# Kernel tuning notes

Hardware: AMD Instinct MI355X
Metric: run time of the kernel (lower is better)

The kernel has to match this reference:

```python
import jax, jax.numpy as jnp
import numpy as np

B, N, D, H = 2, 28, 128, 8
DK = D // H  # 16


def setup_inputs() -> dict:
    key0 = jax.random.key(0)
    ks = jax.random.split(key0, 10)
    query = jax.random.normal(ks[0], (B, N, N, D), dtype=jnp.float32)
    key = jax.random.normal(ks[1], (B, N, N, D), dtype=jnp.float32)
    value = jax.random.normal(ks[2], (B, N, N, D), dtype=jnp.float32)
    mask = jax.random.randint(ks[3], (B, N, N, N), 0, 2).astype(bool)
    scale = 1.0 / np.sqrt(D)
    # six bias-free Linear(d_model, d_model) weights (torch layout: y = x @ W.T)
    Wlk = jax.random.normal(ks[4], (D, D), dtype=jnp.float32) * scale
    Wrk = jax.random.normal(ks[5], (D, D), dtype=jnp.float32) * scale
    Wlv = jax.random.normal(ks[6], (D, D), dtype=jnp.float32) * scale
    Wrv = jax.random.normal(ks[7], (D, D), dtype=jnp.float32) * scale
    Wq = jax.random.normal(ks[8], (D, D), dtype=jnp.float32) * scale
    Wout = jax.random.normal(ks[9], (D, D), dtype=jnp.float32) * scale
    return {"query": query, "key": key, "value": value, "mask": mask,
            "Wlk": Wlk, "Wrk": Wrk, "Wlv": Wlv, "Wrv": Wrv, "Wq": Wq, "Wout": Wout}


def reference(query, key, value, mask, Wlk, Wrk, Wlv, Wrv, Wq, Wout):
    b, n = key.shape[0], key.shape[1]

    def proj(x, W):
        # torch nn.Linear(bias=False): x @ W.T, then view to heads
        return (x @ W.T).reshape(b, n, n, H, DK)

    left_k = proj(key, Wlk)
    right_k = proj(key, Wrk)
    left_v = proj(value, Wlv)
    right_v = proj(value, Wrv)
    # note: linears[4](key) (the 'query' projection, Wq) is computed in the
    # original but unused when lesion_scores=False; omitted (same math).

    # scores[b,x,a,y,h] = <left_k[b,x,a,h,:], right_k[b,a,y,h,:]> / sqrt(d_k)
    scores = jnp.einsum('bxahd,bayhd->bxayh', left_k, right_k) / np.float32(np.sqrt(DK))
    scores = jnp.where(mask[..., None], jnp.float32(-1e9), scores)
    att = jax.nn.softmax(scores, axis=2)  # softmax over intermediate node a
    # dropout p=0.0 -> identity
    # x[b,x,y,h,d] = sum_a att[b,x,a,y,h] * left_v[b,x,a,h,d] * right_v[b,a,y,h,d]
    x = jnp.einsum('bxayh,bxahd,bayhd->bxyhd', att, left_v, right_v)
    x = x.reshape(b, n, n, D)
    return x @ Wout.T
```

## Files before the change

### kernel.cpp

```cpp
#include <hip/hip_runtime.h>

#define B_ 2
#define N_ 28
#define D_ 128
#define H_ 8
#define DK_ 16
#define R_ (B_ * N_ * N_)
#define ROWS_PER_BLK 8

__global__ __launch_bounds__(128) void proj4_kernel(
    const float* __restrict__ key, const float* __restrict__ value,
    const float* __restrict__ Wlk, const float* __restrict__ Wrk,
    const float* __restrict__ Wlv, const float* __restrict__ Wrv,
    float* __restrict__ ws) {
  const int p = blockIdx.y;
  const float* X = (p < 2) ? key : value;
  const float* W = (p == 0) ? Wlk : (p == 1) ? Wrk : (p == 2) ? Wlv : Wrv;
  float* Y = ws + (size_t)p * R_ * D_;

  const int r0 = blockIdx.x * ROWS_PER_BLK;
  const int c = threadIdx.x;

  __shared__ float xs[ROWS_PER_BLK][D_];
#pragma unroll
  for (int i = 0; i < ROWS_PER_BLK; ++i)
    xs[i][c] = X[(size_t)(r0 + i) * D_ + c];
  __syncthreads();

  const float4* w4 = reinterpret_cast<const float4*>(W + (size_t)c * D_);
  float acc[ROWS_PER_BLK];
#pragma unroll
  for (int i = 0; i < ROWS_PER_BLK; ++i) acc[i] = 0.f;

#pragma unroll
  for (int k = 0; k < D_ / 4; ++k) {
    const float4 wv = w4[k];
#pragma unroll
    for (int i = 0; i < ROWS_PER_BLK; ++i) {
      const float4 xv = reinterpret_cast<const float4*>(xs[i])[k];
      acc[i] += xv.x * wv.x + xv.y * wv.y + xv.z * wv.z + xv.w * wv.w;
    }
  }

#pragma unroll
  for (int i = 0; i < ROWS_PER_BLK; ++i)
    Y[(size_t)(r0 + i) * D_ + c] = acc[i];
}

__global__ __launch_bounds__(128) void attn_kernel(
    const float* __restrict__ ws, const int* __restrict__ mask,
    float* __restrict__ xout) {
  const float* lk = ws;
  const float* rk = ws + (size_t)1 * R_ * D_;
  const float* lv = ws + (size_t)2 * R_ * D_;
  const float* rv = ws + (size_t)3 * R_ * D_;

  const int bxy = blockIdx.x;
  const int y = bxy % N_;
  const int bx = bxy / N_;
  const int b = bx / N_;
  const int tid = threadIdx.x;

  const int rowL = bx * N_;
  const int rowR = b * N_ * N_ + y;

  float s[N_];
#pragma unroll
  for (int a = 0; a < N_; ++a) {
    float pr = lk[(size_t)(rowL + a) * D_ + tid] *
               rk[(size_t)(rowR + a * N_) * D_ + tid];
    pr += __shfl_xor(pr, 1);
    pr += __shfl_xor(pr, 2);
    pr += __shfl_xor(pr, 4);
    pr += __shfl_xor(pr, 8);
    s[a] = pr * 0.25f;
  }

  const int* mrow = mask + (size_t)rowL * N_ + y;
#pragma unroll
  for (int a = 0; a < N_; ++a)
    if (mrow[(size_t)a * N_] != 0) s[a] = -1e9f;

  float mx = -3.0e38f;
#pragma unroll
  for (int a = 0; a < N_; ++a) mx = fmaxf(mx, s[a]);
  float den = 0.f;
#pragma unroll
  for (int a = 0; a < N_; ++a) {
    s[a] = __expf(s[a] - mx);
    den += s[a];
  }
  const float inv = 1.0f / den;

  float xv = 0.f;
#pragma unroll
  for (int a = 0; a < N_; ++a) {
    xv += s[a] * lv[(size_t)(rowL + a) * D_ + tid] *
          rv[(size_t)(rowR + a * N_) * D_ + tid];
  }
  xout[(size_t)bxy * D_ + tid] = xv * inv;
}

__global__ __launch_bounds__(128) void gemm_out_kernel(
    const float* __restrict__ X, const float* __restrict__ W,
    float* __restrict__ Y) {
  const int r0 = blockIdx.x * ROWS_PER_BLK;
  const int c = threadIdx.x;

  __shared__ float xs[ROWS_PER_BLK][D_];
#pragma unroll
  for (int i = 0; i < ROWS_PER_BLK; ++i)
    xs[i][c] = X[(size_t)(r0 + i) * D_ + c];
  __syncthreads();

  const float4* w4 = reinterpret_cast<const float4*>(W + (size_t)c * D_);
  float acc[ROWS_PER_BLK];
#pragma unroll
  for (int i = 0; i < ROWS_PER_BLK; ++i) acc[i] = 0.f;

#pragma unroll
  for (int k = 0; k < D_ / 4; ++k) {
    const float4 wv = w4[k];
#pragma unroll
    for (int i = 0; i < ROWS_PER_BLK; ++i) {
      const float4 xv = reinterpret_cast<const float4*>(xs[i])[k];
      acc[i] += xv.x * wv.x + xv.y * wv.y + xv.z * wv.z + xv.w * wv.w;
    }
  }

#pragma unroll
  for (int i = 0; i < ROWS_PER_BLK; ++i)
    Y[(size_t)(r0 + i) * D_ + c] = acc[i];
}

extern "C" void kernel_launch(void* const* d_in, const int* in_sizes, int n_in,
                              void* d_out, int out_size, void* d_ws,
                              size_t ws_size, hipStream_t stream) {
  const float* key = (const float*)d_in[1];
  const float* value = (const float*)d_in[2];
  const int* mask = (const int*)d_in[3];
  const float* Wlk = (const float*)d_in[4];
  const float* Wrk = (const float*)d_in[5];
  const float* Wlv = (const float*)d_in[6];
  const float* Wrv = (const float*)d_in[7];
  const float* Wout = (const float*)d_in[9];
  float* out = (float*)d_out;

  float* ws = (float*)d_ws;
  float* xbuf = ws + (size_t)4 * R_ * D_;

  proj4_kernel<<<dim3(R_ / ROWS_PER_BLK, 4), 128, 0, stream>>>(
      key, value, Wlk, Wrk, Wlv, Wrv, ws);
  attn_kernel<<<dim3(R_), 128, 0, stream>>>(ws, mask, xbuf);
  gemm_out_kernel<<<dim3(R_ / ROWS_PER_BLK), 128, 0, stream>>>(xbuf, Wout, out);
}
```

Before: 33.56 us.

## Fuse attention with output projection and reuse left rows across y group

Merges the attention kernel and the output GEMM into one kernel, so the intermediate x buffer never goes to global memory and one launch is removed. Each block now handles four y values for one (b,x), staging left_k and left_v rows in shared memory once and reusing them. The output projection is done per row, with each thread reading a full Wout row from global memory for every y, and two block barriers per y. The grid shrinks from 1568 to 392 blocks, which lowers parallelism.

```diff
diff --git a/kernel.cpp b/kernel.cpp
--- a/kernel.cpp
+++ b/kernel.cpp
@@ -7,6 +7,7 @@
 #define DK_ 16
 #define R_ (B_ * N_ * N_)
 #define ROWS_PER_BLK 8
+#define YG_ 4
 
 __global__ __launch_bounds__(128) void proj4_kernel(
     const float* __restrict__ key, const float* __restrict__ value,
@@ -47,90 +48,84 @@
     Y[(size_t)(r0 + i) * D_ + c] = acc[i];
 }
 
-__global__ __launch_bounds__(128) void attn_kernel(
+__global__ __launch_bounds__(128) void attn_out_kernel(
     const float* __restrict__ ws, const int* __restrict__ mask,
-    float* __restrict__ xout) {
+    const float* __restrict__ Wout, float* __restrict__ out) {
   const float* lk = ws;
   const float* rk = ws + (size_t)1 * R_ * D_;
   const float* lv = ws + (size_t)2 * R_ * D_;
   const float* rv = ws + (size_t)3 * R_ * D_;
 
-  const int bxy = blockIdx.x;
-  const int y = bxy % N_;
-  const int bx = bxy / N_;
+  const int yg = blockIdx.x % (N_ / YG_);
+  const int bx = blockIdx.x / (N_ / YG_);
   const int b = bx / N_;
   const int tid = threadIdx.x;
 
   const int rowL = bx * N_;
-  const int rowR = b * N_ * N_ + y;
 
-  float s[N_];
+  __shared__ float s_lk[N_][D_];
+  __shared__ float s_lv[N_][D_];
+  __shared__ float s_x[D_];
+
 #pragma unroll
   for (int a = 0; a < N_; ++a) {
-    float pr = lk[(size_t)(rowL + a) * D_ + tid] *
-               rk[(size_t)(rowR + a * N_) * D_ + tid];
-    pr += __shfl_xor(pr, 1);
-    pr += __shfl_xor(pr, 2);
-    pr += __shfl_xor(pr, 4);
-    pr += __shfl_xor(pr, 8);
-    s[a] = pr * 0.25f;
+    s_lk[a][tid] = lk[(size_t)(rowL + a) * D_ + tid];
+    s_lv[a][tid] = lv[(size_t)(rowL + a) * D_ + tid];
   }
-
-  const int* mrow = mask + (size_t)rowL * N_ + y;
-#pragma unroll
-  for (int a = 0; a < N_; ++a)
-    if (mrow[(size_t)a * N_] != 0) s[a] = -1e9f;
-
-  float mx = -3.0e38f;
-#pragma unroll
-  for (int a = 0; a < N_; ++a) mx = fmaxf(mx, s[a]);
-  float den = 0.f;
-#pragma unroll
-  for (int a = 0; a < N_; ++a) {
-    s[a] = __expf(s[a] - mx);
-    den += s[a];
-  }
-  const float inv = 1.0f / den;
-
-  float xv = 0.f;
-#pragma unroll
-  for (int a = 0; a < N_; ++a) {
-    xv += s[a] * lv[(size_t)(rowL + a) * D_ + tid] *
-          rv[(size_t)(rowR + a * N_) * D_ + tid];
-  }
-  xout[(size_t)bxy * D_ + tid] = xv * inv;
-}
-
-__global__ __launch_bounds__(128) void gemm_out_kernel(
-    const float* __restrict__ X, const float* __restrict__ W,
-    float* __restrict__ Y) {
-  const int r0 = blockIdx.x * ROWS_PER_BLK;
-  const int c = threadIdx.x;
-
-  __shared__ float xs[ROWS_PER_BLK][D_];
-#pragma unroll
-  for (int i = 0; i < ROWS_PER_BLK; ++i)
-    xs[i][c] = X[(size_t)(r0 + i) * D_ + c];
   __syncthreads();
 
-  const float4* w4 = reinterpret_cast<const float4*>(W + (size_t)c * D_);
-  float acc[ROWS_PER_BLK];
+  const float4* wrow = reinterpret_cast<const float4*>(Wout + (size_t)tid * D_);
+
+  for (int j = 0; j < YG_; ++j) {
+    const int y = yg * YG_ + j;
+    const int rowR = b * N_ * N_ + y;
+
+    float s[N_];
 #pragma unroll
-  for (int i = 0; i < ROWS_PER_BLK; ++i) acc[i] = 0.f;
+    for (int a = 0; a < N_; ++a) {
+      float pr = s_lk[a][tid] * rk[(size_t)(rowR + a * N_) * D_ + tid];
+      pr += __shfl_xor(pr, 1);
+      pr += __shfl_xor(pr, 2);
+      pr += __shfl_xor(pr, 4);
+      pr += __shfl_xor(pr, 8);
+      s[a] = pr * 0.25f;
+    }
 
+    const int* mrow = mask + (size_t)rowL * N_ + y;
 #pragma unroll
-  for (int k = 0; k < D_ / 4; ++k) {
-    const float4 wv = w4[k];
+    for (int a = 0; a < N_; ++a)
+      if (mrow[(size_t)a * N_] != 0) s[a] = -1e9f;
+
+    float mx = -3.0e38f;
 #pragma unroll
-    for (int i = 0; i < ROWS_PER_BLK; ++i) {
-      const float4 xv = reinterpret_cast<const float4*>(xs[i])[k];
-      acc[i] += xv.x * wv.x + xv.y * wv.y + xv.z * wv.z + xv.w * wv.w;
+    for (int a = 0; a < N_; ++a) mx = fmaxf(mx, s[a]);
+    float den = 0.f;
+#pragma unroll
+    for (int a = 0; a < N_; ++a) {
+      s[a] = __expf(s[a] - mx);
+      den += s[a];
     }
+    const float inv = 1.0f / den;
+
+    float xv = 0.f;
+#pragma unroll
+    for (int a = 0; a < N_; ++a) {
+      xv += s[a] * s_lv[a][tid] * rv[(size_t)(rowR + a * N_) * D_ + tid];
+    }
+    s_x[tid] = xv * inv;
+    __syncthreads();
+
+    float acc = 0.f;
+    const float4* x4 = reinterpret_cast<const float4*>(s_x);
+#pragma unroll
+    for (int k = 0; k < D_ / 4; ++k) {
+      const float4 xk = x4[k];
+      const float4 wv = wrow[k];
+      acc += xk.x * wv.x + xk.y * wv.y + xk.z * wv.z + xk.w * wv.w;
+    }
+    out[(size_t)(rowL + y) * D_ + tid] = acc;
+    __syncthreads();
   }
-
-#pragma unroll
-  for (int i = 0; i < ROWS_PER_BLK; ++i)
-    Y[(size_t)(r0 + i) * D_ + c] = acc[i];
 }
 
 extern "C" void kernel_launch(void* const* d_in, const int* in_sizes, int n_in,
@@ -147,10 +142,9 @@
   float* out = (float*)d_out;
 
   float* ws = (float*)d_ws;
-  float* xbuf = ws + (size_t)4 * R_ * D_;
 
   proj4_kernel<<<dim3(R_ / ROWS_PER_BLK, 4), 128, 0, stream>>>(
       key, value, Wlk, Wrk, Wlv, Wrv, ws);
-  attn_kernel<<<dim3(R_), 128, 0, stream>>>(ws, mask, xbuf);
-  gemm_out_kernel<<<dim3(R_ / ROWS_PER_BLK), 128, 0, stream>>>(xbuf, Wout, out);
+  attn_out_kernel<<<dim3((N_ / YG_) * B_ * N_), 128, 0, stream>>>(ws, mask,
+                                                                  Wout, out);
 }
```

New measurement: 42.16 us. 25.6% more time.

## Remap attention kernel threads to (head, intermediate node) pairs with warp-shuffle softmax

Applied to the files above, without the earlier changes.

The attention kernel now launches 256 threads per output position, each handling one (head, intermediate node a) pair. Each thread computes its score with float4 loads and applies the mask. Softmax and the weighted value sum are done with cross-lane shuffle reductions over 32 lanes, and results are staged through shared memory before the store. This replaces the per-thread serial loop over 28 nodes and its 28 sequential shuffle reductions. In exchange it uses more threads, leaves 4 of every 32 lanes idle, and adds 20 shuffle reductions per lane for the value accumulation.

```diff
diff --git a/kernel.cpp b/kernel.cpp
--- a/kernel.cpp
+++ b/kernel.cpp
@@ -1,4 +1,5 @@
 #include <hip/hip_runtime.h>
+#include <math.h>
 
 #define B_ 2
 #define N_ 28
@@ -21,7 +22,7 @@
   const int r0 = blockIdx.x * ROWS_PER_BLK;
   const int c = threadIdx.x;
 
-  __shared__ float xs[ROWS_PER_BLK][D_];
+  __shared__ __align__(16) float xs[ROWS_PER_BLK][D_];
 #pragma unroll
   for (int i = 0; i < ROWS_PER_BLK; ++i)
     xs[i][c] = X[(size_t)(r0 + i) * D_ + c];
@@ -47,7 +48,7 @@
     Y[(size_t)(r0 + i) * D_ + c] = acc[i];
 }
 
-__global__ __launch_bounds__(128) void attn_kernel(
+__global__ __launch_bounds__(256) void attn_kernel(
     const float* __restrict__ ws, const int* __restrict__ mask,
     float* __restrict__ xout) {
   const float* lk = ws;
@@ -59,46 +60,75 @@
   const int y = bxy % N_;
   const int bx = bxy / N_;
   const int b = bx / N_;
+
   const int tid = threadIdx.x;
+  const int h = tid >> 5;
+  const int a = tid & 31;
+  const bool act = (a < N_);
+  const int al = act ? a : (N_ - 1);
 
   const int rowL = bx * N_;
   const int rowR = b * N_ * N_ + y;
 
-  float s[N_];
+  const float4* lk4 =
+      reinterpret_cast<const float4*>(lk + (size_t)(rowL + al) * D_ + h * DK_);
+  const float4* rk4 = reinterpret_cast<const float4*>(
+      rk + (size_t)(rowR + al * N_) * D_ + h * DK_);
+  float s = 0.f;
 #pragma unroll
-  for (int a = 0; a < N_; ++a) {
-    float pr = lk[(size_t)(rowL + a) * D_ + tid] *
-               rk[(size_t)(rowR + a * N_) * D_ + tid];
-    pr += __shfl_xor(pr, 1);
-    pr += __shfl_xor(pr, 2);
-    pr += __shfl_xor(pr, 4);
-    pr += __shfl_xor(pr, 8);
-    s[a] = pr * 0.25f;
+  for (int j = 0; j < 4; ++j) {
+    const float4 u = lk4[j];
+    const float4 v = rk4[j];
+    s += u.x * v.x + u.y * v.y + u.z * v.z + u.w * v.w;
+  }
+  s *= 0.25f;
+
+  if (act && mask[(size_t)(rowL + a) * N_ + y] != 0) s = -1e9f;
+  if (!act) s = -INFINITY;
+
+  float mx = s;
+#pragma unroll
+  for (int m = 1; m <= 16; m <<= 1) mx = fmaxf(mx, __shfl_xor(mx, m));
+  float e = __expf(s - mx);
+  float den = e;
+#pragma unroll
+  for (int m = 1; m <= 16; m <<= 1) den += __shfl_xor(den, m);
+  const float att = e / den;
+
+  const float4* lv4 =
+      reinterpret_cast<const float4*>(lv + (size_t)(rowL + al) * D_ + h * DK_);
+  const float4* rv4 = reinterpret_cast<const float4*>(
+      rv + (size_t)(rowR + al * N_) * D_ + h * DK_);
+  float4 acc[4];
+#pragma unroll
+  for (int j = 0; j < 4; ++j) {
+    const float4 u = lv4[j];
+    const float4 v = rv4[j];
+    acc[j].x = att * u.x * v.x;
+    acc[j].y = att * u.y * v.y;
+    acc[j].z = att * u.z * v.z;
+    acc[j].w = att * u.w * v.w;
+  }
+#pragma unroll
+  for (int m = 1; m <= 16; m <<= 1) {
+#pragma unroll
+    for (int j = 0; j < 4; ++j) {
+      acc[j].x += __shfl_xor(acc[j].x, m);
+      acc[j].y += __shfl_xor(acc[j].y, m);
+      acc[j].z += __shfl_xor(acc[j].z, m);
+      acc[j].w += __shfl_xor(acc[j].w, m);
+    }
   }
 
-  const int* mrow = mask + (size_t)rowL * N_ + y;
+  __shared__ __align__(16) float s_x[D_];
+  if (a == 0) {
+    float4* dst = reinterpret_cast<float4*>(s_x + h * DK_);
 #pragma unroll
-  for (int a = 0; a < N_; ++a)
-    if (mrow[(size_t)a * N_] != 0) s[a] = -1e9f;
+    for (int j = 0; j < 4; ++j) dst[j] = acc[j];
+  }
+  __syncthreads();
 
-  float mx = -3.0e38f;
-#pragma unroll
-  for (int a = 0; a < N_; ++a) mx = fmaxf(mx, s[a]);
-  float den = 0.f;
-#pragma unroll
-  for (int a = 0; a < N_; ++a) {
-    s[a] = __expf(s[a] - mx);
-    den += s[a];
-  }
-  const float inv = 1.0f / den;
-
-  float xv = 0.f;
-#pragma unroll
-  for (int a = 0; a < N_; ++a) {
-    xv += s[a] * lv[(size_t)(rowL + a) * D_ + tid] *
-          rv[(size_t)(rowR + a * N_) * D_ + tid];
-  }
-  xout[(size_t)bxy * D_ + tid] = xv * inv;
+  if (tid < D_) xout[(size_t)bxy * D_ + tid] = s_x[tid];
 }
 
 __global__ __launch_bounds__(128) void gemm_out_kernel(
@@ -107,7 +137,7 @@
   const int r0 = blockIdx.x * ROWS_PER_BLK;
   const int c = threadIdx.x;
 
-  __shared__ float xs[ROWS_PER_BLK][D_];
+  __shared__ __align__(16) float xs[ROWS_PER_BLK][D_];
 #pragma unroll
   for (int i = 0; i < ROWS_PER_BLK; ++i)
     xs[i][c] = X[(size_t)(r0 + i) * D_ + c];
@@ -145,12 +175,11 @@
   const float* Wrv = (const float*)d_in[7];
   const float* Wout = (const float*)d_in[9];
   float* out = (float*)d_out;
-
   float* ws = (float*)d_ws;
   float* xbuf = ws + (size_t)4 * R_ * D_;
 
   proj4_kernel<<<dim3(R_ / ROWS_PER_BLK, 4), 128, 0, stream>>>(
       key, value, Wlk, Wrk, Wlv, Wrv, ws);
-  attn_kernel<<<dim3(R_), 128, 0, stream>>>(ws, mask, xbuf);
+  attn_kernel<<<dim3(R_), 256, 0, stream>>>(ws, mask, xbuf);
   gemm_out_kernel<<<dim3(R_ / ROWS_PER_BLK), 128, 0, stream>>>(xbuf, Wout, out);
 }
```

New measurement: 39.94 us. 1.19x slower.
